# Performance work log

Measured on AMD Instinct MI355X. Metric: run time of the kernel, lower is better.

## Reference

```python
import jax, jax.numpy as jnp
import numpy as np

K = 5          # deformable kernel size
PAD = 2        # deformable conv padding
K3 = K * K * K


def conv3d(x, w, b, pad, dil=1, groups=1):
    out = jax.lax.conv_general_dilated(
        x, w, (1, 1, 1), [(pad, pad)] * 3,
        rhs_dilation=(dil, dil, dil),
        dimension_numbers=('NCDHW', 'OIDHW', 'NCDHW'),
        feature_group_count=groups)
    return out + b[None, :, None, None, None]


def deform_depthwise_conv3d(x, offsets, w_dw, b_dw):
    # x: [B,C,D,H,W], offsets: [B,3*K3,D,H,W] (per kernel tap: (dz,dy,dx))
    B, C, D, H, W = x.shape
    off = offsets.reshape(B, K3, 3, D, H, W)
    kz, ky, kx = jnp.meshgrid(jnp.arange(K), jnp.arange(K), jnp.arange(K), indexing='ij')
    kgrid = jnp.stack([kz, ky, kx], -1).reshape(K3, 3).astype(x.dtype)  # [K3,3]
    gd = jnp.arange(D, dtype=x.dtype)[None, :, None, None]
    gh = jnp.arange(H, dtype=x.dtype)[None, None, :, None]
    gw = jnp.arange(W, dtype=x.dtype)[None, None, None, :]
    # sampling coords per kernel tap: p0 - pad + k + learned offset -> [B,K3,D,H,W]
    pd = gd - PAD + kgrid[:, 0][:, None, None, None] + off[:, :, 0]
    ph = gh - PAD + kgrid[:, 1][:, None, None, None] + off[:, :, 1]
    pw = gw - PAD + kgrid[:, 2][:, None, None, None] + off[:, :, 2]

    def sample_one(xb, pdb, phb, pwb):
        # xb: [C,D,H,W]; coords: [K3,D,H,W] -> trilinear sample, zero pad outside
        d0 = jnp.floor(pdb); h0 = jnp.floor(phb); w0 = jnp.floor(pwb)
        fd = pdb - d0; fh = phb - h0; fw = pwb - w0
        acc = jnp.zeros((C,) + pdb.shape, xb.dtype)
        for dd in (0, 1):
            wd = fd if dd else 1.0 - fd
            di = d0 + dd
            for hh in (0, 1):
                wh = fh if hh else 1.0 - fh
                hi = h0 + hh
                for ww in (0, 1):
                    wgt = wd * wh * (fw if ww else 1.0 - fw)
                    wi = w0 + ww
                    valid = ((di >= 0) & (di < D) & (hi >= 0) & (hi < H)
                             & (wi >= 0) & (wi < W)).astype(xb.dtype)
                    ii = jnp.clip(di, 0, D - 1).astype(jnp.int32)
                    jj = jnp.clip(hi, 0, H - 1).astype(jnp.int32)
                    kk = jnp.clip(wi, 0, W - 1).astype(jnp.int32)
                    v = xb[:, ii, jj, kk]  # [C,K3,D,H,W]
                    acc = acc + v * (wgt * valid)[None]
        return acc

    val = jax.vmap(sample_one)(x, pd, ph, pw)            # [B,C,K3,D,H,W]
    out = jnp.einsum('bckdhw,ck->bcdhw', val, w_dw.reshape(C, K3))
    return out + b_dw[None, :, None, None, None]


def setup_inputs():
    key = jax.random.key(0)
    ks = jax.random.split(key, 9)
    B, C, S = 1, 32, 20
    x = jax.random.normal(ks[0], (B, C, S, S, S), jnp.float32)
    w_off = jax.random.normal(ks[1], (3 * K3, C, K, K, K), jnp.float32) * 0.01
    b_off = jnp.zeros((3 * K3,), jnp.float32)
    w_dw = jax.random.normal(ks[2], (C, 1, K, K, K), jnp.float32) * 0.1
    b_dw = jax.random.normal(ks[3], (C,), jnp.float32) * 0.1
    w_sp = jax.random.normal(ks[4], (C, 1, 7, 7, 7), jnp.float32) * 0.05
    b_sp = jax.random.normal(ks[5], (C,), jnp.float32) * 0.1
    w_pw = jax.random.normal(ks[6], (C, C), jnp.float32) * 0.1
    b_pw = jax.random.normal(ks[7], (C,), jnp.float32) * 0.1
    return {'x': x, 'w_off': w_off, 'b_off': b_off, 'w_dw': w_dw, 'b_dw': b_dw,
            'w_sp': w_sp, 'b_sp': b_sp, 'w_pw': w_pw, 'b_pw': b_pw}


def reference(x, w_off, b_off, w_dw, b_dw, w_sp, b_sp, w_pw, b_pw):
    C = x.shape[1]
    # DeformConvPack: offset conv (same geometry as main conv), then deformable depthwise conv
    offsets = conv3d(x, w_off, b_off, PAD)
    attn = deform_depthwise_conv3d(x, offsets, w_dw, b_dw)
    # dilated depthwise 7x7x7, dilation 3, padding 9 (size preserving)
    attn = conv3d(attn, w_sp, b_sp, 9, dil=3, groups=C)
    # pointwise 1x1x1 conv
    attn = jnp.einsum('oc,bcdhw->bodhw', w_pw, attn) + b_pw[None, :, None, None, None]
    return x * attn
```

## Files before the change

kernel.cpp:

```cpp
#include <hip/hip_runtime.h>
#include <hip/hip_bf16.h>

#define C_   32
#define S_   20
#define V_   8000
#define K3_  125
#define OC_  375
#define NP_  384
#define KK_  4000

#define WS_ATTN1T 0
#define WS_XT     256000
#define WS_WDWT   384000
#define WS_WSPT   388000
#define WS_WPWT   398976
#define WS_OFFB   400000
#define WS_BPREP  1936000
#define WS_XP     1936000
#define WS_ZERO   WS_ATTN1T

typedef __attribute__((ext_vector_type(8))) short bf16x8;
typedef __attribute__((ext_vector_type(4))) float f32x4;
typedef __fp16 h2_t __attribute__((ext_vector_type(2)));

static __device__ __forceinline__ unsigned short f2h(float f) {
    _Float16 h = (_Float16)f;
    return __builtin_bit_cast(unsigned short, h);
}
static __device__ __forceinline__ float h2f(unsigned short b) {
    return (float)__builtin_bit_cast(_Float16, b);
}
static __device__ __forceinline__ h2_t bch2(unsigned u) {
    return __builtin_bit_cast(h2_t, u);
}
static __device__ __forceinline__ unsigned pkh2(float a, float b) {
#if __has_builtin(__builtin_amdgcn_cvt_pkrtz)
    return __builtin_bit_cast(unsigned, __builtin_amdgcn_cvt_pkrtz(a, b));
#else
    return (unsigned)f2h(a) | ((unsigned)f2h(b) << 16);
#endif
}
static __device__ __forceinline__ float dot2(unsigned xu, unsigned wu, float c) {
#if __has_builtin(__builtin_amdgcn_fdot2)
    return __builtin_amdgcn_fdot2(bch2(xu), bch2(wu), c, false);
#else
    h2_t xh = bch2(xu), wh = bch2(wu);
    return c + (float)xh[0] * (float)wh[0] + (float)xh[1] * (float)wh[1];
#endif
}

__global__ __launch_bounds__(256) void transpose_kernel(
    const float* __restrict__ x,
    const float* __restrict__ w_dw,
    const float* __restrict__ w_sp,
    const float* __restrict__ w_pw,
    unsigned short* __restrict__ xt,
    float* __restrict__ wdwT,
    float* __restrict__ wspT,
    float* __restrict__ wpwT,
    float* __restrict__ zpage)
{
    int i = blockIdx.x * 256 + threadIdx.x;
    if (i < 256000) {
        int v = i >> 5, c = i & 31;
        xt[i] = f2h(x[c * V_ + v]);
        return;
    }
    int j = i - 256000;
    if (j < 4000)  { wdwT[j] = w_dw[(j & 31) * K3_ + (j >> 5)]; return; }
    j -= 4000;
    if (j < 10976) { wspT[j] = w_sp[(j & 31) * 343 + (j >> 5)]; return; }
    j -= 10976;
    if (j < 1024)  { wpwT[j] = w_pw[(j & 31) * 32 + (j >> 5)]; return; }
    j -= 1024;
    if (j < 16)    { zpage[j] = 0.f; return; }
}

__global__ __launch_bounds__(256) void prep_b_kernel(
    const float* __restrict__ w_off, unsigned short* __restrict__ Bprep)
{
    int idx = blockIdx.x * 256 + threadIdx.x;
    if (idx >= NP_ * KK_) return;
    int n = idx / KK_, r = idx % KK_;
    int tap = r >> 5, c = r & 31;
    float v = (n < OC_) ? w_off[n * KK_ + c * K3_ + tap] : 0.f;
    Bprep[idx] = f2h(v);
}

__global__ __launch_bounds__(256) void gemm_off_kernel(
    const unsigned short* __restrict__ xt,
    const unsigned short* __restrict__ Bprep,
    const float* __restrict__ b_off,
    const float* __restrict__ zpage,
    unsigned short* __restrict__ offbT)
{
    __shared__ unsigned short A_lds[2][2][64 * 32];
    __shared__ unsigned short B_lds[2][2][64 * 32];

    const int t    = threadIdx.x;
    const int lane = t & 63;
    const int wave = t >> 6;
    const int wr   = wave >> 1;
    const int wc   = wave & 1;
    const int quad = lane >> 4;
    const int lrow = lane & 15;
    const int M0   = blockIdx.x * 64;
    const int N0   = blockIdx.y * 64;

    const int srow = t >> 2;
    const int soff = ((t & 3) ^ ((t >> 3) & 3)) * 8;
    const int mg = M0 + srow;
    const int az = mg / 400, arm = mg % 400;
    const int ay = arm / 20, ax = arm % 20;
    const unsigned short* brow = Bprep + (size_t)(N0 + srow) * KK_;
    const unsigned short* zp   = (const unsigned short*)zpage;
    const int ldsoff = wave * 512;
    const int xorc = (lrow >> 1) & 3;

    f32x4 acc[2][2] = {};

    auto stage = [&](int buf, int tap0) {
        #pragma unroll
        for (int h = 0; h < 2; ++h) {
            int tap = tap0 + h;
            int kz = tap / 25, ky = (tap / 5) % 5, kx = tap % 5;
            int zi = az - 2 + kz, yi = ay - 2 + ky, xi = ax - 2 + kx;
            bool intap = tap < K3_;
            bool ok = intap & ((unsigned)zi < (unsigned)S_)
                            & ((unsigned)yi < (unsigned)S_)
                            & ((unsigned)xi < (unsigned)S_);
            int px = zi * 400 + yi * 20 + xi;
            const unsigned short* ga = ok    ? (xt + px * 32 + soff)    : zp;
            const unsigned short* gb = intap ? (brow + tap * 32 + soff) : zp;
            __builtin_amdgcn_global_load_lds(
                (const __attribute__((address_space(1))) void*)ga,
                (__attribute__((address_space(3))) void*)(&A_lds[buf][h][ldsoff]),
                16, 0, 0);
            __builtin_amdgcn_global_load_lds(
                (const __attribute__((address_space(1))) void*)gb,
                (__attribute__((address_space(3))) void*)(&B_lds[buf][h][ldsoff]),
                16, 0, 0);
        }
    };

    stage(0, 0);
    __syncthreads();

    int cur = 0;
    for (int it = 0; it < 63; ++it) {
        if (it < 62) stage(cur ^ 1, (it + 1) * 2);
        #pragma unroll
        for (int h = 0; h < 2; ++h) {
            bf16x8 af[2], bf[2];
            #pragma unroll
            for (int mi = 0; mi < 2; ++mi)
                af[mi] = *(const bf16x8*)&A_lds[cur][h][(wr * 32 + mi * 16 + lrow) * 32 + (quad ^ xorc) * 8];
            #pragma unroll
            for (int ni = 0; ni < 2; ++ni)
                bf[ni] = *(const bf16x8*)&B_lds[cur][h][(wc * 32 + ni * 16 + lrow) * 32 + (quad ^ xorc) * 8];
            #pragma unroll
            for (int mi = 0; mi < 2; ++mi)
                #pragma unroll
                for (int ni = 0; ni < 2; ++ni)
                    acc[mi][ni] = __builtin_amdgcn_mfma_f32_16x16x32_f16(
                        af[mi], bf[ni], acc[mi][ni], 0, 0, 0);
        }
        __syncthreads();
        cur ^= 1;
    }

    #pragma unroll
    for (int mi = 0; mi < 2; ++mi) {
        #pragma unroll
        for (int ni = 0; ni < 2; ++ni) {
            int n = N0 + wc * 32 + ni * 16 + lrow;
            if (n < OC_) {
                float bias = b_off[n];
                #pragma unroll
                for (int r = 0; r < 4; ++r) {
                    int row = wr * 32 + mi * 16 + quad * 4 + r;
                    offbT[(size_t)(M0 + row) * 384 + n] = f2h(acc[mi][ni][r] + bias);
                }
            }
        }
    }
}

__global__ __launch_bounds__(256) void pack_xp_kernel(
    const unsigned short* __restrict__ xt, unsigned* __restrict__ xp)
{
    int i = blockIdx.x * 256 + threadIdx.x;
    if (i >= 256000) return;
    unsigned lo = xt[i];
    unsigned hi = (i < 256000 - 32) ? (unsigned)xt[i + 32] : 0u;
    xp[i] = lo | (hi << 16);
}

#define VB 8
__global__ __launch_bounds__(256) void deform_kernel(
    const unsigned* __restrict__ xp,
    const float* __restrict__ wdwT,
    const float* __restrict__ b_dw,
    const unsigned short* __restrict__ offbT,
    float* __restrict__ attn1T)
{
    __shared__ unsigned sw[VB * 128 * 8];
    const int tid = threadIdx.x;
    const int Vb = blockIdx.x * VB;

    for (int idx = tid; idx < VB * 128; idx += 256) {
        int vl = idx >> 7, tap = idx & 127;
        if (tap < K3_) {
            int v = Vb + vl;
            int z = v / 400, rm = v % 400;
            int y = rm / 20, xx = rm % 20;
            int kz = tap / 25, ky = (tap / 5) % 5, kx = tap % 5;
            const unsigned short* ob = offbT + v * 384 + 3 * tap;
            float pd = (float)(z - 2 + kz) + h2f(ob[0]);
            float ph = (float)(y - 2 + ky) + h2f(ob[1]);
            float pw = (float)(xx - 2 + kx) + h2f(ob[2]);
            float fd0 = floorf(pd), fh0 = floorf(ph), fw0 = floorf(pw);
            float fd = pd - fd0, fh = ph - fh0, fw = pw - fw0;
            int id = (int)fd0, ih = (int)fh0, iw = (int)fw0;
            int d0 = min(max(id, 0), S_ - 1), d1 = min(max(id + 1, 0), S_ - 1);
            int h0 = min(max(ih, 0), S_ - 1), h1 = min(max(ih + 1, 0), S_ - 1);
            float wd0 = ((unsigned)id       < (unsigned)S_) ? 1.f - fd : 0.f;
            float wd1 = ((unsigned)(id + 1) < (unsigned)S_) ? fd       : 0.f;
            float wh0 = ((unsigned)ih       < (unsigned)S_) ? 1.f - fh : 0.f;
            float wh1 = ((unsigned)(ih + 1) < (unsigned)S_) ? fh       : 0.f;
            float ww0 = ((unsigned)iw       < (unsigned)S_) ? 1.f - fw : 0.f;
            float ww1 = ((unsigned)(iw + 1) < (unsigned)S_) ? fw       : 0.f;
            int px; float wwa, wwb;
            if (iw < 0) { px = 0;             wwa = ww1; wwb = 0.f; }
            else        { px = min(iw, S_-1); wwa = ww0; wwb = ww1; }
            int r00 = d0 * 400 + h0 * 20 + px;
            int r01 = d0 * 400 + h1 * 20 + px;
            int r10 = d1 * 400 + h0 * 20 + px;
            int r11 = d1 * 400 + h1 * 20 + px;
            float w00 = wd0 * wh0, w01 = wd0 * wh1;
            float w10 = wd1 * wh0, w11 = wd1 * wh1;
            unsigned* q = &sw[idx * 8];
            q[0] = pkh2(w00 * wwa, w00 * wwb);
            q[1] = pkh2(w01 * wwa, w01 * wwb);
            q[2] = pkh2(w10 * wwa, w10 * wwb);
            q[3] = pkh2(w11 * wwa, w11 * wwb);
            q[4] = (unsigned)r00 | ((unsigned)r01 << 16);
            q[5] = (unsigned)r10 | ((unsigned)r11 << 16);
        }
    }
    __syncthreads();

    const int c = tid & 31;
    const int vl = tid >> 5;
    const int v = Vb + vl;
    const unsigned* xpc = xp + c;
    float acc = 0.f;
    #pragma unroll 4
    for (int tap = 0; tap < K3_; ++tap) {
        const unsigned* q = &sw[(vl * 128 + tap) * 8];
        unsigned w00u = q[0], w01u = q[1], w10u = q[2], w11u = q[3];
        unsigned pA = q[4], pB = q[5];
        int p00 = pA & 0xFFFFu, p01 = pA >> 16;
        int p10 = pB & 0xFFFFu, p11 = pB >> 16;
        float s = dot2(xpc[p00 * 32], w00u,
                  dot2(xpc[p01 * 32], w01u,
                  dot2(xpc[p10 * 32], w10u,
                  dot2(xpc[p11 * 32], w11u, 0.f))));
        acc += wdwT[tap * 32 + c] * s;
    }
    attn1T[v * 32 + c] = acc + b_dw[c];
}

__global__ __launch_bounds__(256) void spatial_pw_kernel(
    const float* __restrict__ wspT,
    const float* __restrict__ b_sp,
    const float* __restrict__ attn1T,
    const float* __restrict__ wpwT,
    const float* __restrict__ b_pw,
    const float* __restrict__ x,
    float* __restrict__ out)
{
    __shared__ float s_attn[8][32];
    int t = threadIdx.x;
    int c = t & 31;
    int vl = t >> 5;
    int v = blockIdx.x * 8 + vl;
    int z = v / 400, rm = v % 400;
    int y = rm / 20, xx = rm % 20;

    float acc = 0.f;
    #pragma unroll 1
    for (int kz = 0; kz < 7; ++kz) {
        int zi = z - 9 + 3 * kz;
        bool zv = (unsigned)zi < (unsigned)S_;
        int zc2 = min(max(zi, 0), S_ - 1);
        #pragma unroll 1
        for (int ky = 0; ky < 7; ++ky) {
            int yi = y - 9 + 3 * ky;
            bool yv = (unsigned)yi < (unsigned)S_;
            int yc2 = min(max(yi, 0), S_ - 1);
            int abase = (zc2 * 400 + yc2 * 20) * 32 + c;
            int wbase = (kz * 49 + ky * 7) * 32 + c;
            #pragma unroll
            for (int kx = 0; kx < 7; ++kx) {
                int xi = xx - 9 + 3 * kx;
                bool xv = (unsigned)xi < (unsigned)S_;
                int xc2 = min(max(xi, 0), S_ - 1);
                float a = attn1T[abase + xc2 * 32];
                float w = wspT[wbase + kx * 32];
                acc += (zv && yv && xv) ? a * w : 0.f;
            }
        }
    }
    s_attn[vl][c] = acc + b_sp[c];
    __syncthreads();

    const int o = c;
    float acc2 = b_pw[o];
    #pragma unroll
    for (int cc = 0; cc < C_; ++cc)
        acc2 += wpwT[cc * 32 + o] * s_attn[vl][cc];
    out[o * V_ + v] = x[o * V_ + v] * acc2;
}

extern "C" void kernel_launch(void* const* d_in, const int* in_sizes, int n_in,
                              void* d_out, int out_size, void* d_ws, size_t ws_size,
                              hipStream_t stream)
{
    const float* x     = (const float*)d_in[0];
    const float* w_off = (const float*)d_in[1];
    const float* b_off = (const float*)d_in[2];
    const float* w_dw  = (const float*)d_in[3];
    const float* b_dw  = (const float*)d_in[4];
    const float* w_sp  = (const float*)d_in[5];
    const float* b_sp  = (const float*)d_in[6];
    const float* w_pw  = (const float*)d_in[7];
    const float* b_pw  = (const float*)d_in[8];
    float* ws = (float*)d_ws;
    float* out = (float*)d_out;

    unsigned short* xt    = (unsigned short*)(ws + WS_XT);
    unsigned short* offbT = (unsigned short*)(ws + WS_OFFB);
    unsigned short* Bprep = (unsigned short*)(ws + WS_BPREP);
    unsigned*       xp    = (unsigned*)(ws + WS_XP);

    hipLaunchKernelGGL(transpose_kernel, dim3((272016 + 255) / 256), dim3(256), 0, stream,
                       x, w_dw, w_sp, w_pw, xt,
                       ws + WS_WDWT, ws + WS_WSPT, ws + WS_WPWT, ws + WS_ZERO);

    hipLaunchKernelGGL(prep_b_kernel, dim3((NP_ * KK_ + 255) / 256), dim3(256), 0, stream,
                       w_off, Bprep);

    hipLaunchKernelGGL(gemm_off_kernel, dim3(125, 6), dim3(256), 0, stream,
                       xt, Bprep, b_off, ws + WS_ZERO, offbT);

    hipLaunchKernelGGL(pack_xp_kernel, dim3(1000), dim3(256), 0, stream,
                       xt, xp);

    hipLaunchKernelGGL(deform_kernel, dim3(1000), dim3(256), 0, stream,
                       xp, ws + WS_WDWT, b_dw, offbT, ws + WS_ATTN1T);

    hipLaunchKernelGGL(spatial_pw_kernel, dim3(1000), dim3(256), 0, stream,
                       ws + WS_WSPT, b_sp, ws + WS_ATTN1T,
                       ws + WS_WPWT, b_pw, x, out);
}
```

Measured before the change: 191.1 us.

## Tile transposes through LDS and clip dilated-conv loop bounds to valid taps

The x transpose and the offset-weight repack now stage data in shared memory, so both the global reads and the global writes are coalesced instead of strided. The dilated 7x7x7 depthwise conv computes per-voxel tap bounds and skips out-of-range taps, which removes the clamping, predication and wasted loads at the borders. In exchange the inner loops are no longer fully unrolled, and the trip count now varies per thread, which adds some divergence within a wave.

```diff
diff --git a/kernel.cpp b/kernel.cpp
--- a/kernel.cpp
+++ b/kernel.cpp
@@ -60,13 +60,30 @@
     float* __restrict__ wpwT,
     float* __restrict__ zpage)
 {
-    int i = blockIdx.x * 256 + threadIdx.x;
-    if (i < 256000) {
-        int v = i >> 5, c = i & 31;
-        xt[i] = f2h(x[c * V_ + v]);
+    const int tid = threadIdx.x;
+    if (blockIdx.x < 125) {
+        __shared__ float tile[32][65];
+        const int v0 = blockIdx.x * 64;
+        {
+            int vv = tid & 63, cc = tid >> 6;
+            #pragma unroll
+            for (int p = 0; p < 8; ++p) {
+                int c = cc + p * 4;
+                tile[c][vv] = x[c * V_ + v0 + vv];
+            }
+        }
+        __syncthreads();
+        {
+            int c = tid & 31, vl = tid >> 5;
+            #pragma unroll
+            for (int p = 0; p < 8; ++p) {
+                int v = vl + p * 8;
+                xt[(v0 + v) * 32 + c] = f2h(tile[c][v]);
+            }
+        }
         return;
     }
-    int j = i - 256000;
+    int j = (blockIdx.x - 125) * 256 + tid;
     if (j < 4000)  { wdwT[j] = w_dw[(j & 31) * K3_ + (j >> 5)]; return; }
     j -= 4000;
     if (j < 10976) { wspT[j] = w_sp[(j & 31) * 343 + (j >> 5)]; return; }
@@ -79,12 +96,17 @@
 __global__ __launch_bounds__(256) void prep_b_kernel(
     const float* __restrict__ w_off, unsigned short* __restrict__ Bprep)
 {
-    int idx = blockIdx.x * 256 + threadIdx.x;
-    if (idx >= NP_ * KK_) return;
-    int n = idx / KK_, r = idx % KK_;
-    int tap = r >> 5, c = r & 31;
-    float v = (n < OC_) ? w_off[n * KK_ + c * K3_ + tap] : 0.f;
-    Bprep[idx] = f2h(v);
+    __shared__ float tile[KK_];
+    const int n = blockIdx.x;
+    const int tid = threadIdx.x;
+    const bool live = n < OC_;
+    for (int i = tid; i < KK_; i += 256)
+        tile[i] = live ? w_off[(size_t)n * KK_ + i] : 0.f;
+    __syncthreads();
+    for (int j = tid; j < KK_; j += 256) {
+        int tap = j >> 5, c = j & 31;
+        Bprep[(size_t)n * KK_ + j] = f2h(tile[c * K3_ + tap]);
+    }
 }
 
 __global__ __launch_bounds__(256) void gemm_off_kernel(
@@ -288,27 +310,22 @@
     int z = v / 400, rm = v % 400;
     int y = rm / 20, xx = rm % 20;
 
+    int kz_lo = max(0, (11 - z) / 3), kz_hi = min(6, (28 - z) / 3);
+    int ky_lo = max(0, (11 - y) / 3), ky_hi = min(6, (28 - y) / 3);
+    int kx_lo = max(0, (11 - xx) / 3), kx_hi = min(6, (28 - xx) / 3);
+
     float acc = 0.f;
     #pragma unroll 1
-    for (int kz = 0; kz < 7; ++kz) {
+    for (int kz = kz_lo; kz <= kz_hi; ++kz) {
         int zi = z - 9 + 3 * kz;
-        bool zv = (unsigned)zi < (unsigned)S_;
-        int zc2 = min(max(zi, 0), S_ - 1);
         #pragma unroll 1
-        for (int ky = 0; ky < 7; ++ky) {
+        for (int ky = ky_lo; ky <= ky_hi; ++ky) {
             int yi = y - 9 + 3 * ky;
-            bool yv = (unsigned)yi < (unsigned)S_;
-            int yc2 = min(max(yi, 0), S_ - 1);
-            int abase = (zc2 * 400 + yc2 * 20) * 32 + c;
+            int abase = (zi * 400 + yi * 20 + (xx - 9)) * 32 + c;
             int wbase = (kz * 49 + ky * 7) * 32 + c;
-            #pragma unroll
-            for (int kx = 0; kx < 7; ++kx) {
-                int xi = xx - 9 + 3 * kx;
-                bool xv = (unsigned)xi < (unsigned)S_;
-                int xc2 = min(max(xi, 0), S_ - 1);
-                float a = attn1T[abase + xc2 * 32];
-                float w = wspT[wbase + kx * 32];
-                acc += (zv && yv && xv) ? a * w : 0.f;
+            #pragma unroll 1
+            for (int kx = kx_lo; kx <= kx_hi; ++kx) {
+                acc += attn1T[abase + 3 * kx * 32] * wspT[wbase + kx * 32];
             }
         }
     }
@@ -344,11 +361,11 @@
     unsigned short* Bprep = (unsigned short*)(ws + WS_BPREP);
     unsigned*       xp    = (unsigned*)(ws + WS_XP);
 
-    hipLaunchKernelGGL(transpose_kernel, dim3((272016 + 255) / 256), dim3(256), 0, stream,
+    hipLaunchKernelGGL(transpose_kernel, dim3(188), dim3(256), 0, stream,
                        x, w_dw, w_sp, w_pw, xt,
                        ws + WS_WDWT, ws + WS_WSPT, ws + WS_WPWT, ws + WS_ZERO);
 
-    hipLaunchKernelGGL(prep_b_kernel, dim3((NP_ * KK_ + 255) / 256), dim3(256), 0, stream,
+    hipLaunchKernelGGL(prep_b_kernel, dim3(NP_), dim3(256), 0, stream,
                        w_off, Bprep);
 
     hipLaunchKernelGGL(gemm_off_kernel, dim3(125, 6), dim3(256), 0, stream,
```

Result: slower. 213.3 us (+11.6%).
